# Performance work log

Hardware: AMD Instinct MI355X
Metric: run time of the kernel (lower is better)

## Reference

```python
import jax, jax.numpy as jnp
import numpy as np

N = 32768      # nodes
E = 262144     # edges
G = 256        # graphs
D_IN, D_H, D_OUT = 256, 512, 512
STEPS = 3      # set2set processing steps


def setup_inputs() -> dict:
    key = jax.random.key(0)
    ks = jax.random.split(key, 10)
    x = jax.random.normal(ks[0], (N, D_IN), jnp.float32)
    edge_index = jax.random.randint(ks[1], (2, E), 0, N, dtype=jnp.int64)
    batch = jnp.sort(jax.random.randint(ks[2], (N,), 0, G, dtype=jnp.int64))
    W1 = jax.random.normal(ks[3], (D_IN, D_H), jnp.float32) * (1.0 / np.sqrt(D_IN))
    b1 = jnp.zeros((D_H,), jnp.float32)
    W2 = jax.random.normal(ks[4], (D_H, D_OUT), jnp.float32) * (1.0 / np.sqrt(D_H))
    b2 = jnp.zeros((D_OUT,), jnp.float32)
    # LSTM(input=2*D_OUT, hidden=D_OUT); gate order i,f,g,o (PyTorch)
    s = 1.0 / np.sqrt(D_OUT)
    W_ih = jax.random.uniform(ks[5], (4 * D_OUT, 2 * D_OUT), jnp.float32, -s, s)
    W_hh = jax.random.uniform(ks[6], (4 * D_OUT, D_OUT), jnp.float32, -s, s)
    b_ih = jax.random.uniform(ks[7], (4 * D_OUT,), jnp.float32, -s, s)
    b_hh = jax.random.uniform(ks[8], (4 * D_OUT,), jnp.float32, -s, s)
    return {"x": x, "edge_index": edge_index, "batch": batch,
            "W1": W1, "b1": b1, "W2": W2, "b2": b2,
            "W_ih": W_ih, "W_hh": W_hh, "b_ih": b_ih, "b_hh": b_hh}


def _gcn_conv(x, src, dst, norm, W, b):
    # GCNConv: symmetric-normalized aggregation of linearly transformed features
    h = x @ W                              # [N, d_out]
    msg = h[src] * norm[:, None]           # gather + scale  [E+N, d_out]
    agg = jax.ops.segment_sum(msg, dst, num_segments=N)
    return agg + b


def reference(x, edge_index, batch, W1, b1, W2, b2, W_ih, W_hh, b_ih, b_hh):
    # --- GCN normalization with self-loops: D^-1/2 (A+I) D^-1/2 ---
    loop = jnp.arange(N, dtype=edge_index.dtype)
    src = jnp.concatenate([edge_index[0], loop])
    dst = jnp.concatenate([edge_index[1], loop])
    deg = jax.ops.segment_sum(jnp.ones_like(src, x.dtype), dst, num_segments=N)
    dinv = jax.lax.rsqrt(deg)              # deg >= 1 thanks to self-loops
    norm = dinv[src] * dinv[dst]

    h = jax.nn.relu(_gcn_conv(x, src, dst, norm, W1, b1))
    h = _gcn_conv(h, src, dst, norm, W2, b2)   # [N, D_OUT]

    # --- Set2Set pooling (3 processing steps) ---
    d = D_OUT
    q_star = jnp.zeros((G, 2 * d), h.dtype)
    hs = jnp.zeros((G, d), h.dtype)
    cs = jnp.zeros((G, d), h.dtype)
    for _ in range(STEPS):
        gates = q_star @ W_ih.T + b_ih + hs @ W_hh.T + b_hh
        i, f, g, o = jnp.split(gates, 4, axis=-1)
        cs = jax.nn.sigmoid(f) * cs + jax.nn.sigmoid(i) * jnp.tanh(g)
        hs = jax.nn.sigmoid(o) * jnp.tanh(cs)      # query q  [G, d]
        e = jnp.sum(h * hs[batch], axis=-1)        # [N]
        emax = jax.ops.segment_max(e, batch, num_segments=G)
        emax = jnp.where(jnp.isfinite(emax), emax, 0.0)
        ex = jnp.exp(e - emax[batch])
        denom = jax.ops.segment_sum(ex, batch, num_segments=G)
        a = ex / jnp.maximum(denom, 1e-12)[batch]  # per-graph softmax
        r = jax.ops.segment_sum(a[:, None] * h, batch, num_segments=G)
        q_star = jnp.concatenate([hs, r], axis=-1)  # [G, 2d]
    return q_star
```

## Files before the change

### kernel.cpp

```cpp
#include <hip/hip_runtime.h>
#include <math.h>

#define NN 32768
#define NE 262144
#define NG 256
#define DIN 256
#define DH 512
#define DOUT 512

typedef unsigned short u16;
typedef _Float16 f16;
typedef __attribute__((ext_vector_type(4))) _Float16 f16x4;
typedef __attribute__((ext_vector_type(8))) _Float16 f16x8;
typedef __attribute__((ext_vector_type(4))) float f32x4;

__device__ inline void split2h(float f, f16& h, f16& l) {
  h = (f16)f;
  l = (f16)(f - (float)h);
}

__device__ inline void gload16(const void* g, void* l) {
  __builtin_amdgcn_global_load_lds((const __attribute__((address_space(1))) unsigned int*)g,
                                   (__attribute__((address_space(3))) unsigned int*)l,
                                   16, 0, 0);
}


__global__ __launch_bounds__(128) void k_scanA(const int* __restrict__ counts,
                                               int* __restrict__ bsum) {
  int b = blockIdx.x, t = threadIdx.x;
  int v = counts[b * 128 + t];
  __shared__ int red[128];
  red[t] = v;
  __syncthreads();
#pragma unroll
  for (int o = 64; o > 0; o >>= 1) {
    if (t < o) red[t] += red[t + o];
    __syncthreads();
  }
  if (t == 0) bsum[b] = red[0];
}

__global__ __launch_bounds__(256) void k_scanB(const int* __restrict__ bsum,
                                               int* __restrict__ boff,
                                               int* __restrict__ offs) {
  __shared__ int s[256];
  int t = threadIdx.x;
  int v = bsum[t];
  s[t] = v;
  __syncthreads();
  for (int o = 1; o < 256; o <<= 1) {
    int add = (t >= o) ? s[t - o] : 0;
    __syncthreads();
    s[t] += add;
    __syncthreads();
  }
  boff[t] = s[t] - v;
  if (t == 255) offs[NN] = s[255];
}

__global__ __launch_bounds__(128) void k_scanC(const int* __restrict__ counts,
                                               const int* __restrict__ boff,
                                               int* __restrict__ offs,
                                               float* __restrict__ dinv) {
  int b = blockIdx.x, t = threadIdx.x;
  int v = counts[b * 128 + t];
  __shared__ int s[128];
  s[t] = v;
  __syncthreads();
  for (int o = 1; o < 128; o <<= 1) {
    int add = (t >= o) ? s[t - o] : 0;
    __syncthreads();
    s[t] += add;
    __syncthreads();
  }
  offs[b * 128 + t] = boff[b] + s[t] - v;
  dinv[b * 128 + t] = rsqrtf((float)(v + 1));
}

__global__ void k_fill(const int* __restrict__ ei, const int* __restrict__ offs,
                       int* __restrict__ cursor, int* __restrict__ csr) {
  int e = blockIdx.x * 256 + threadIdx.x;
  if (e < NE) {
    int d = ei[NE + e];
    int pos = offs[d] + atomicAdd(&cursor[d], 1);
    csr[pos] = ei[e];
  }
}

__global__ void k_prep(const float* __restrict__ x, f16* __restrict__ xh,
                       const float* __restrict__ W1, f16* __restrict__ w1th,
                       const float* __restrict__ W2, f16* __restrict__ w2th,
                       const float* __restrict__ W_ih, const float* __restrict__ W_hh,
                       f16* __restrict__ wgh,
                       const int* __restrict__ batch, int* __restrict__ starts,
                       const int* __restrict__ ei, int* __restrict__ counts) {
  int b = blockIdx.x;
  if (b < 8192) {
    int i = (b * 256 + threadIdx.x) << 2;
    float4 v = *(const float4*)(x + i);
    f16x4 h = {(f16)v.x, (f16)v.y, (f16)v.z, (f16)v.w};
    *(f16x4*)(xh + i) = h;
  } else if (b < 8704) {
    int idx = (b - 8192) * 256 + threadIdx.x;
    int k = idx >> 9, n = idx & 511;
    w1th[(size_t)n * DIN + k] = (f16)W1[idx];
  } else if (b < 9728) {
    int idx = (b - 8704) * 256 + threadIdx.x;
    int k = idx >> 9, n = idx & 511;
    w2th[(size_t)n * DH + k] = (f16)W2[idx];
  } else if (b < 17920) {
    int idx = (b - 9728) * 256 + threadIdx.x;
    int n = idx >> 10, c = idx & 1023;
    float v = W_ih[(size_t)n * 1024 + c];
    if (c < 512) v += W_hh[(size_t)n * 512 + c];
    wgh[idx] = (f16)v;
  } else if (b == 17920) {
    int g = threadIdx.x;
    int lo = 0, hi = NN;
    while (lo < hi) {
      int mid = (lo + hi) >> 1;
      if (batch[mid] < g) lo = mid + 1; else hi = mid;
    }
    starts[g] = lo;
    if (g == 0) starts[NG] = NN;
  } else {
    int e = (b - 17921) * 256 + threadIdx.x;
    if (e < NE) atomicAdd(&counts[ei[NE + e]], 1);
  }
}

template <int MODE, int TERMS>
__global__ __launch_bounds__(256) void k_mfma_gemm(
    const f16* __restrict__ Ahi, const f16* __restrict__ Alo,
    const f16* __restrict__ Bhi,
    float* __restrict__ C, f16* __restrict__ Cf16, const float* __restrict__ bias,
    int M, int N, int K, int lda, int ldb) {
  constexpr int BOFF = (TERMS == 2) ? 32768 : 16384;
  __shared__ char lds[(TERMS == 2) ? 49152 : 32768];

  int nbn = N >> 7;
  int nwg = (M >> 7) * nbn;
  int b = blockIdx.x;
  int slice = b / nwg;
  b -= slice * nwg;
  int koff = slice * K;
  int swz = (b & 7) * (nwg >> 3) + (b >> 3);
  int bn = (swz % nbn) << 7;
  int bm = (swz / nbn) << 7;

  int tid = threadIdx.x;
  int w = tid >> 6, lane = tid & 63;
  int wm = (w >> 1) << 6, wn = (w & 1) << 6;
  int fr = lane & 15;
  int fq = lane >> 4;

  f32x4 acc[4][4];
#pragma unroll
  for (int i = 0; i < 4; ++i)
#pragma unroll
    for (int j = 0; j < 4; ++j) acc[i][j] = (f32x4){0.f, 0.f, 0.f, 0.f};

  for (int ks = 0; ks < K; ks += 64) {
#pragma unroll
    for (int i = 0; i < 4; ++i) {
      int L = i * 256 + tid;
      int row = L >> 3;
      int ke = ((L & 7) ^ (row & 7)) << 3;
      int ldsoff = i * 4096 + w * 1024;
      gload16(Ahi + (size_t)(bm + row) * lda + koff + ks + ke, lds + ldsoff);
      if (TERMS == 2)
        gload16(Alo + (size_t)(bm + row) * lda + koff + ks + ke, lds + 16384 + ldsoff);
      gload16(Bhi + (size_t)(bn + row) * ldb + koff + ks + ke, lds + BOFF + ldsoff);
    }
    __syncthreads();
#pragma unroll
    for (int kk = 0; kk < 2; ++kk) {
      f16x8 ah[4], al[4], bh[4];
#pragma unroll
      for (int m = 0; m < 4; ++m) {
        int row = wm + m * 16 + fr;
        int boff = row * 128 + (((kk << 6) + (fq << 4)) ^ ((row & 7) << 4));
        ah[m] = *(const f16x8*)(lds + boff);
        if (TERMS == 2) al[m] = *(const f16x8*)(lds + 16384 + boff);
      }
#pragma unroll
      for (int n = 0; n < 4; ++n) {
        int row = wn + n * 16 + fr;
        int boff = row * 128 + (((kk << 6) + (fq << 4)) ^ ((row & 7) << 4));
        bh[n] = *(const f16x8*)(lds + BOFF + boff);
      }
#pragma unroll
      for (int m = 0; m < 4; ++m)
#pragma unroll
        for (int n = 0; n < 4; ++n) {
          acc[m][n] = __builtin_amdgcn_mfma_f32_16x16x32_f16(ah[m], bh[n], acc[m][n], 0, 0, 0);
          if (TERMS == 2)
            acc[m][n] = __builtin_amdgcn_mfma_f32_16x16x32_f16(al[m], bh[n], acc[m][n], 0, 0, 0);
        }
    }
    __syncthreads();
  }
#pragma unroll
  for (int m = 0; m < 4; ++m)
#pragma unroll
    for (int n = 0; n < 4; ++n)
#pragma unroll
      for (int i = 0; i < 4; ++i) {
        int r = bm + wm + m * 16 + fq * 4 + i;
        int c = bn + wn + n * 16 + fr;
        float val = acc[m][n][i];
        if (MODE == 1) {
          val += bias[c];
          val = fmaxf(val, 0.f);
          Cf16[(size_t)r * N + c] = (f16)val;
        } else if (MODE == 2) {
          Cf16[(size_t)r * N + c] = (f16)val;
        } else {
          C[(size_t)slice * M * N + (size_t)r * N + c] = val;
        }
      }
}

__global__ __launch_bounds__(256) void k_agg256(const f16* __restrict__ xh,
                                                const int* __restrict__ offs,
                                                const int* __restrict__ csr,
                                                const float* __restrict__ dinv,
                                                f16* __restrict__ oh) {
  int wv = threadIdx.x >> 6, lane = threadIdx.x & 63;
  int v = blockIdx.x * 4 + wv;
  int f = lane << 2;
  int s = offs[v], t = offs[v + 1];
  float dv = dinv[v];
  f16x4 rs = *(const f16x4*)(xh + (size_t)v * DIN + f);
  float a0[4] = {}, a1[4] = {}, a2[4] = {}, a3[4] = {};
  for (int base = s; base < t; base += 64) {
    int rem = min(64, t - base);
    int idx = (lane < rem) ? csr[base + lane] : 0;
    float wl = (lane < rem) ? dinv[idx] : 0.f;
    int i = 0;
    for (; i + 7 < rem; i += 8) {
      int u[8]; float ww[8]; f16x4 r[8];
#pragma unroll
      for (int q = 0; q < 8; ++q) { u[q] = __shfl(idx, i + q); ww[q] = __shfl(wl, i + q); }
#pragma unroll
      for (int q = 0; q < 8; ++q) r[q] = *(const f16x4*)(xh + (size_t)u[q] * DIN + f);
#pragma unroll
      for (int k = 0; k < 4; ++k) {
        a0[k] += ww[0] * (float)r[0][k]; a1[k] += ww[1] * (float)r[1][k];
        a2[k] += ww[2] * (float)r[2][k]; a3[k] += ww[3] * (float)r[3][k];
        a0[k] += ww[4] * (float)r[4][k]; a1[k] += ww[5] * (float)r[5][k];
        a2[k] += ww[6] * (float)r[6][k]; a3[k] += ww[7] * (float)r[7][k];
      }
    }
    for (; i + 1 < rem; i += 2) {
      int u0 = __shfl(idx, i), u1 = __shfl(idx, i + 1);
      float w0 = __shfl(wl, i), w1 = __shfl(wl, i + 1);
      f16x4 r0 = *(const f16x4*)(xh + (size_t)u0 * DIN + f);
      f16x4 r1 = *(const f16x4*)(xh + (size_t)u1 * DIN + f);
#pragma unroll
      for (int k = 0; k < 4; ++k) { a0[k] += w0 * (float)r0[k]; a1[k] += w1 * (float)r1[k]; }
    }
    if (i < rem) {
      int u0 = __shfl(idx, i);
      float w0 = __shfl(wl, i);
      f16x4 r0 = *(const f16x4*)(xh + (size_t)u0 * DIN + f);
#pragma unroll
      for (int k = 0; k < 4; ++k) a0[k] += w0 * (float)r0[k];
    }
  }
  f16x4 vh;
#pragma unroll
  for (int k = 0; k < 4; ++k)
    vh[k] = (f16)((a0[k] + a1[k] + a2[k] + a3[k] + dv * (float)rs[k]) * dv);
  *(f16x4*)(oh + (size_t)v * DIN + f) = vh;
}

__global__ __launch_bounds__(256) void k_agg512(const f16* __restrict__ T2,
                                                const int* __restrict__ offs,
                                                const int* __restrict__ csr,
                                                const float* __restrict__ dinv,
                                                const float* __restrict__ bias,
                                                f16* __restrict__ H2) {
  int half = blockIdx.x / (NN / 4);
  int blk = blockIdx.x - half * (NN / 4);
  int wv = threadIdx.x >> 6, lane = threadIdx.x & 63;
  int v = blk * 4 + wv;
  int f = half * 256 + (lane << 2);
  int s = offs[v], t = offs[v + 1];
  float dv = dinv[v];
  f16x4 rs = *(const f16x4*)(T2 + (size_t)v * DH + f);
  float a0[4] = {}, a1[4] = {}, a2[4] = {}, a3[4] = {};
  for (int base = s; base < t; base += 64) {
    int rem = min(64, t - base);
    int idx = (lane < rem) ? csr[base + lane] : 0;
    float wl = (lane < rem) ? dinv[idx] : 0.f;
    int i = 0;
    for (; i + 7 < rem; i += 8) {
      int u[8]; float ww[8]; f16x4 r[8];
#pragma unroll
      for (int q = 0; q < 8; ++q) { u[q] = __shfl(idx, i + q); ww[q] = __shfl(wl, i + q); }
#pragma unroll
      for (int q = 0; q < 8; ++q) r[q] = *(const f16x4*)(T2 + (size_t)u[q] * DH + f);
#pragma unroll
      for (int k = 0; k < 4; ++k) {
        a0[k] += ww[0] * (float)r[0][k]; a1[k] += ww[1] * (float)r[1][k];
        a2[k] += ww[2] * (float)r[2][k]; a3[k] += ww[3] * (float)r[3][k];
        a0[k] += ww[4] * (float)r[4][k]; a1[k] += ww[5] * (float)r[5][k];
        a2[k] += ww[6] * (float)r[6][k]; a3[k] += ww[7] * (float)r[7][k];
      }
    }
    for (; i + 1 < rem; i += 2) {
      int u0 = __shfl(idx, i), u1 = __shfl(idx, i + 1);
      float w0 = __shfl(wl, i), w1 = __shfl(wl, i + 1);
      f16x4 r0 = *(const f16x4*)(T2 + (size_t)u0 * DH + f);
      f16x4 r1 = *(const f16x4*)(T2 + (size_t)u1 * DH + f);
#pragma unroll
      for (int k = 0; k < 4; ++k) { a0[k] += w0 * (float)r0[k]; a1[k] += w1 * (float)r1[k]; }
    }
    if (i < rem) {
      int u0 = __shfl(idx, i);
      float w0 = __shfl(wl, i);
      f16x4 r0 = *(const f16x4*)(T2 + (size_t)u0 * DH + f);
#pragma unroll
      for (int k = 0; k < 4; ++k) a0[k] += w0 * (float)r0[k];
    }
  }
  float4 bb = *(const float4*)(bias + f);
  float bbv[4] = {bb.x, bb.y, bb.z, bb.w};
  f16x4 out;
#pragma unroll
  for (int k = 0; k < 4; ++k)
    out[k] = (f16)((a0[k] + a1[k] + a2[k] + a3[k] + dv * (float)rs[k]) * dv + bbv[k]);
  *(f16x4*)(H2 + (size_t)v * DH + f) = out;
}

template <int STEP0>
__global__ __launch_bounds__(512) void k_step(const float* __restrict__ gp,
                                              const float* __restrict__ b_ih,
                                              const float* __restrict__ b_hh,
                                              float* __restrict__ cs,
                                              const f16* __restrict__ H2,
                                              const int* __restrict__ starts,
                                              float* __restrict__ qstar,
                                              f16* __restrict__ qhhi, f16* __restrict__ qhlo) {
  int g = blockIdx.x;
  int tid = threadIdx.x, wv = tid >> 6, lane = tid & 63;
  __shared__ float shs[512];
  __shared__ float lm[8], lsum[8];
  __shared__ float lr[8][512];

  {
    int j = tid;
    float iv = b_ih[j]        + b_hh[j];
    float fv = b_ih[512 + j]  + b_hh[512 + j];
    float gv = b_ih[1024 + j] + b_hh[1024 + j];
    float ov = b_ih[1536 + j] + b_hh[1536 + j];
    if (!STEP0) {
      const float* g0 = gp + (size_t)g * 2048;
#pragma unroll
      for (int sl = 0; sl < 8; ++sl) {
        const float* gs = g0 + (size_t)sl * 524288;
        iv += gs[j]; fv += gs[512 + j]; gv += gs[1024 + j]; ov += gs[1536 + j];
      }
    }
    float si = 1.f / (1.f + expf(-iv));
    float sf = 1.f / (1.f + expf(-fv));
    float so = 1.f / (1.f + expf(-ov));
    float cprev = STEP0 ? 0.f : cs[(size_t)g * 512 + j];
    float c = sf * cprev + si * tanhf(gv);
    float h = so * tanhf(c);
    cs[(size_t)g * 512 + j] = c;
    shs[j] = h;
    qstar[(size_t)g * 1024 + j] = h;
    f16 hh, hl;
    split2h(h, hh, hl);
    qhhi[(size_t)g * 1024 + j] = hh;
    qhlo[(size_t)g * 1024 + j] = hl;
  }
  __syncthreads();

  int s = starts[g], t = starts[g + 1];
  int cnt = t - s;
  float hsr[8];
#pragma unroll
  for (int k = 0; k < 8; ++k) hsr[k] = shs[lane * 8 + k];

  float m = -INFINITY, ssum = 0.f;
  float racc[8] = {};
  f16x8 rv = {};
  if (wv < cnt) rv = *(const f16x8*)(H2 + (size_t)(s + wv) * DH + lane * 8);
  for (int i = wv; i < cnt; i += 8) {
    f16x8 cur = rv;
    if (i + 8 < cnt) rv = *(const f16x8*)(H2 + (size_t)(s + i + 8) * DH + lane * 8);
    float e = 0.f;
#pragma unroll
    for (int k = 0; k < 8; ++k) e += (float)cur[k] * hsr[k];
#pragma unroll
    for (int o = 1; o < 64; o <<= 1) e += __shfl_xor(e, o);
    float mn = fmaxf(m, e);
    float scale = expf(m - mn);
    float p = expf(e - mn);
    ssum = ssum * scale + p;
#pragma unroll
    for (int k = 0; k < 8; ++k) racc[k] = racc[k] * scale + p * (float)cur[k];
    m = mn;
  }
  if (lane == 0) { lm[wv] = m; lsum[wv] = ssum; }
#pragma unroll
  for (int k = 0; k < 8; ++k) lr[wv][lane * 8 + k] = racc[k];
  __syncthreads();
  float M = -INFINITY;
#pragma unroll
  for (int w2 = 0; w2 < 8; ++w2) M = fmaxf(M, lm[w2]);
  if (!(M > -3.0e38f)) M = 0.f;
  float denom = 0.f;
  float sc[8];
#pragma unroll
  for (int w2 = 0; w2 < 8; ++w2) { sc[w2] = expf(lm[w2] - M); denom += lsum[w2] * sc[w2]; }
  float inv = 1.f / fmaxf(denom, 1e-12f);
  int f = tid;
  float r = 0.f;
#pragma unroll
  for (int w2 = 0; w2 < 8; ++w2) r += lr[w2][f] * sc[w2];
  r *= inv;
  qstar[(size_t)g * 1024 + 512 + f] = r;
  f16 h0, l0;
  split2h(r, h0, l0);
  qhhi[(size_t)g * 1024 + 512 + f] = h0;
  qhlo[(size_t)g * 1024 + 512 + f] = l0;
}

extern "C" void kernel_launch(void* const* d_in, const int* in_sizes, int n_in,
                              void* d_out, int out_size, void* d_ws, size_t ws_size,
                              hipStream_t stream) {
  const float* x     = (const float*)d_in[0];
  const int*   ei    = (const int*)d_in[1];
  const int*   batch = (const int*)d_in[2];
  const float* W1    = (const float*)d_in[3];
  const float* b1    = (const float*)d_in[4];
  const float* W2    = (const float*)d_in[5];
  const float* b2    = (const float*)d_in[6];
  const float* W_ih  = (const float*)d_in[7];
  const float* W_hh  = (const float*)d_in[8];
  const float* b_ih  = (const float*)d_in[9];
  const float* b_hh  = (const float*)d_in[10];
  float* qstar = (float*)d_out;

  char* w = (char*)d_ws;
  size_t off = 0;
  auto carve = [&](size_t bytes) -> void* {
    void* p = w + off;
    off += (bytes + 255) & ~(size_t)255;
    return p;
  };
  f16* xh      = (f16*)carve((size_t)NN * DIN * 2);
  f16* axh     = (f16*)carve((size_t)NN * DIN * 2);
  f16* h1h     = (f16*)carve((size_t)NN * DH * 2);
  f16* t2h     = (f16*)carve((size_t)NN * DH * 2);
  f16* H2h     = (f16*)carve((size_t)NN * DH * 2);
  f16* w1th    = (f16*)carve((size_t)DH * DIN * 2);
  f16* w2th    = (f16*)carve((size_t)DH * DH * 2);
  f16* wgh     = (f16*)carve((size_t)2048 * 1024 * 2);
  float* gp    = (float*)carve((size_t)8 * NG * 2048 * 4);
  int* counts  = (int*)carve((size_t)NN * 4);
  int* cursor  = (int*)carve((size_t)NN * 4);
  float* cs    = (float*)carve((size_t)NG * DOUT * 4);
  f16* qhhi    = (f16*)carve((size_t)NG * 1024 * 2);
  f16* qhlo    = (f16*)carve((size_t)NG * 1024 * 2);
  int* offs    = (int*)carve((size_t)(NN + 1) * 4);
  int* csr     = (int*)carve((size_t)NE * 4);
  float* dinv  = (float*)carve((size_t)NN * 4);
  int* starts  = (int*)carve((size_t)(NG + 1) * 4);
  int* bsum    = (int*)carve((size_t)256 * 4);
  int* boff    = (int*)carve((size_t)256 * 4);

  hipMemsetAsync(counts, 0, (size_t)2 * NN * 4, stream);

  k_prep<<<18945, 256, 0, stream>>>(x, xh, W1, w1th, W2, w2th, W_ih, W_hh, wgh,
                                    batch, starts, ei, counts);
  k_scanA<<<NN / 128, 128, 0, stream>>>(counts, bsum);
  k_scanB<<<1, 256, 0, stream>>>(bsum, boff, offs);
  k_scanC<<<NN / 128, 128, 0, stream>>>(counts, boff, offs, dinv);
  k_fill<<<NE / 256, 256, 0, stream>>>(ei, offs, cursor, csr);

  k_agg256<<<NN / 4, 256, 0, stream>>>(xh, offs, csr, dinv, axh);
  k_mfma_gemm<1, 1><<<(NN / 128) * (DH / 128), 256, 0, stream>>>(
      axh, nullptr, w1th, nullptr, h1h, b1, NN, DH, DIN, DIN, DIN);
  k_mfma_gemm<2, 1><<<(NN / 128) * (DH / 128), 256, 0, stream>>>(
      h1h, nullptr, w2th, nullptr, t2h, nullptr, NN, DH, DH, DH, DH);
  k_agg512<<<NN / 2, 256, 0, stream>>>(t2h, offs, csr, dinv, b2, H2h);

  k_step<1><<<NG, 512, 0, stream>>>(nullptr, b_ih, b_hh, cs, H2h, starts, qstar, qhhi, qhlo);
  for (int step = 1; step < 3; ++step) {
    k_mfma_gemm<0, 2><<<8 * (NG / 128) * (2048 / 128), 256, 0, stream>>>(
        qhhi, qhlo, wgh, gp, nullptr, nullptr, NG, 2048, 128, 1024, 1024);
    k_step<0><<<NG, 512, 0, stream>>>(gp, b_ih, b_hh, cs, H2h, starts, qstar, qhhi, qhlo);
  }
}
```

Baseline: 223.9 us.

## Fuse Set2Set steps into one cooperative kernel and merge scan kernels

Replaces the five Set2Set launches (step kernels plus split-K gate GEMMs) with one cooperative kernel that uses grid-wide syncs, with all 256 blocks doing both the gate GEMM slice and the attention step. It also merges the three-kernel prefix scan into one kernel that recomputes each block's prefix by summing all earlier counts, and deepens the H2 prefetch to two rows. The aim is to cut launch overhead and small-kernel tails. In exchange it adds grid.sync cost, leaves half the threads idle in the GEMM phase, and makes the scan do redundant quadratic reads.

```diff
diff --git a/kernel.cpp b/kernel.cpp
--- a/kernel.cpp
+++ b/kernel.cpp
@@ -1,5 +1,8 @@
 #include <hip/hip_runtime.h>
+#include <hip/hip_cooperative_groups.h>
 #include <math.h>
+
+namespace cg = cooperative_groups;
 
 #define NN 32768
 #define NE 262144
@@ -23,69 +26,6 @@
   __builtin_amdgcn_global_load_lds((const __attribute__((address_space(1))) unsigned int*)g,
                                    (__attribute__((address_space(3))) unsigned int*)l,
                                    16, 0, 0);
-}
-
-
-__global__ __launch_bounds__(128) void k_scanA(const int* __restrict__ counts,
-                                               int* __restrict__ bsum) {
-  int b = blockIdx.x, t = threadIdx.x;
-  int v = counts[b * 128 + t];
-  __shared__ int red[128];
-  red[t] = v;
-  __syncthreads();
-#pragma unroll
-  for (int o = 64; o > 0; o >>= 1) {
-    if (t < o) red[t] += red[t + o];
-    __syncthreads();
-  }
-  if (t == 0) bsum[b] = red[0];
-}
-
-__global__ __launch_bounds__(256) void k_scanB(const int* __restrict__ bsum,
-                                               int* __restrict__ boff,
-                                               int* __restrict__ offs) {
-  __shared__ int s[256];
-  int t = threadIdx.x;
-  int v = bsum[t];
-  s[t] = v;
-  __syncthreads();
-  for (int o = 1; o < 256; o <<= 1) {
-    int add = (t >= o) ? s[t - o] : 0;
-    __syncthreads();
-    s[t] += add;
-    __syncthreads();
-  }
-  boff[t] = s[t] - v;
-  if (t == 255) offs[NN] = s[255];
-}
-
-__global__ __launch_bounds__(128) void k_scanC(const int* __restrict__ counts,
-                                               const int* __restrict__ boff,
-                                               int* __restrict__ offs,
-                                               float* __restrict__ dinv) {
-  int b = blockIdx.x, t = threadIdx.x;
-  int v = counts[b * 128 + t];
-  __shared__ int s[128];
-  s[t] = v;
-  __syncthreads();
-  for (int o = 1; o < 128; o <<= 1) {
-    int add = (t >= o) ? s[t - o] : 0;
-    __syncthreads();
-    s[t] += add;
-    __syncthreads();
-  }
-  offs[b * 128 + t] = boff[b] + s[t] - v;
-  dinv[b * 128 + t] = rsqrtf((float)(v + 1));
-}
-
-__global__ void k_fill(const int* __restrict__ ei, const int* __restrict__ offs,
-                       int* __restrict__ cursor, int* __restrict__ csr) {
-  int e = blockIdx.x * 256 + threadIdx.x;
-  if (e < NE) {
-    int d = ei[NE + e];
-    int pos = offs[d] + atomicAdd(&cursor[d], 1);
-    csr[pos] = ei[e];
-  }
 }
 
 __global__ void k_prep(const float* __restrict__ x, f16* __restrict__ xh,
@@ -130,21 +70,60 @@
   }
 }
 
-template <int MODE, int TERMS>
+__global__ __launch_bounds__(256) void k_scan_all(const int* __restrict__ counts,
+                                                  int* __restrict__ offs,
+                                                  float* __restrict__ dinv) {
+  int b = blockIdx.x, tid = threadIdx.x;
+  int limit = b * 128;
+  __shared__ int red[256];
+  int ssum = 0;
+  for (int i = tid; i < limit; i += 256) ssum += counts[i];
+  red[tid] = ssum;
+  __syncthreads();
+#pragma unroll
+  for (int o = 128; o > 0; o >>= 1) {
+    if (tid < o) red[tid] += red[tid + o];
+    __syncthreads();
+  }
+  int prefix = red[0];
+  __syncthreads();
+  __shared__ int s[128];
+  int v = 0;
+  if (tid < 128) { v = counts[limit + tid]; s[tid] = v; }
+  __syncthreads();
+  for (int o = 1; o < 128; o <<= 1) {
+    int add = (tid >= o && tid < 128) ? s[tid - o] : 0;
+    __syncthreads();
+    if (tid < 128) s[tid] += add;
+    __syncthreads();
+  }
+  if (tid < 128) {
+    offs[limit + tid] = prefix + s[tid] - v;
+    dinv[limit + tid] = rsqrtf((float)(v + 1));
+  }
+  if (b == 255 && tid == 127) offs[NN] = prefix + s[127];
+}
+
+__global__ void k_fill(const int* __restrict__ ei, const int* __restrict__ offs,
+                       int* __restrict__ cursor, int* __restrict__ csr) {
+  int e = blockIdx.x * 256 + threadIdx.x;
+  if (e < NE) {
+    int d = ei[NE + e];
+    int pos = offs[d] + atomicAdd(&cursor[d], 1);
+    csr[pos] = ei[e];
+  }
+}
+
+template <int MODE>
 __global__ __launch_bounds__(256) void k_mfma_gemm(
-    const f16* __restrict__ Ahi, const f16* __restrict__ Alo,
-    const f16* __restrict__ Bhi,
-    float* __restrict__ C, f16* __restrict__ Cf16, const float* __restrict__ bias,
+    const f16* __restrict__ A, const f16* __restrict__ B,
+    f16* __restrict__ Cf16, const float* __restrict__ bias,
     int M, int N, int K, int lda, int ldb) {
-  constexpr int BOFF = (TERMS == 2) ? 32768 : 16384;
-  __shared__ char lds[(TERMS == 2) ? 49152 : 32768];
+  __shared__ char lds[32768];
 
   int nbn = N >> 7;
   int nwg = (M >> 7) * nbn;
   int b = blockIdx.x;
-  int slice = b / nwg;
-  b -= slice * nwg;
-  int koff = slice * K;
   int swz = (b & 7) * (nwg >> 3) + (b >> 3);
   int bn = (swz % nbn) << 7;
   int bm = (swz / nbn) << 7;
@@ -168,36 +147,30 @@
       int row = L >> 3;
       int ke = ((L & 7) ^ (row & 7)) << 3;
       int ldsoff = i * 4096 + w * 1024;
-      gload16(Ahi + (size_t)(bm + row) * lda + koff + ks + ke, lds + ldsoff);
-      if (TERMS == 2)
-        gload16(Alo + (size_t)(bm + row) * lda + koff + ks + ke, lds + 16384 + ldsoff);
-      gload16(Bhi + (size_t)(bn + row) * ldb + koff + ks + ke, lds + BOFF + ldsoff);
+      gload16(A + (size_t)(bm + row) * lda + ks + ke, lds + ldsoff);
+      gload16(B + (size_t)(bn + row) * ldb + ks + ke, lds + 16384 + ldsoff);
     }
     __syncthreads();
 #pragma unroll
     for (int kk = 0; kk < 2; ++kk) {
-      f16x8 ah[4], al[4], bh[4];
+      f16x8 ah[4], bh[4];
 #pragma unroll
       for (int m = 0; m < 4; ++m) {
         int row = wm + m * 16 + fr;
         int boff = row * 128 + (((kk << 6) + (fq << 4)) ^ ((row & 7) << 4));
         ah[m] = *(const f16x8*)(lds + boff);
-        if (TERMS == 2) al[m] = *(const f16x8*)(lds + 16384 + boff);
       }
 #pragma unroll
       for (int n = 0; n < 4; ++n) {
         int row = wn + n * 16 + fr;
         int boff = row * 128 + (((kk << 6) + (fq << 4)) ^ ((row & 7) << 4));
-        bh[n] = *(const f16x8*)(lds + BOFF + boff);
+        bh[n] = *(const f16x8*)(lds + 16384 + boff);
       }
 #pragma unroll
       for (int m = 0; m < 4; ++m)
 #pragma unroll
-        for (int n = 0; n < 4; ++n) {
+        for (int n = 0; n < 4; ++n)
           acc[m][n] = __builtin_amdgcn_mfma_f32_16x16x32_f16(ah[m], bh[n], acc[m][n], 0, 0, 0);
-          if (TERMS == 2)
-            acc[m][n] = __builtin_amdgcn_mfma_f32_16x16x32_f16(al[m], bh[n], acc[m][n], 0, 0, 0);
-        }
     }
     __syncthreads();
   }
@@ -213,12 +186,8 @@
         if (MODE == 1) {
           val += bias[c];
           val = fmaxf(val, 0.f);
-          Cf16[(size_t)r * N + c] = (f16)val;
-        } else if (MODE == 2) {
-          Cf16[(size_t)r * N + c] = (f16)val;
-        } else {
-          C[(size_t)slice * M * N + (size_t)r * N + c] = val;
         }
+        Cf16[(size_t)r * N + c] = (f16)val;
       }
 }
 
@@ -335,100 +304,186 @@
   *(f16x4*)(H2 + (size_t)v * DH + f) = out;
 }
 
-template <int STEP0>
-__global__ __launch_bounds__(512) void k_step(const float* __restrict__ gp,
-                                              const float* __restrict__ b_ih,
-                                              const float* __restrict__ b_hh,
-                                              float* __restrict__ cs,
-                                              const f16* __restrict__ H2,
-                                              const int* __restrict__ starts,
-                                              float* __restrict__ qstar,
-                                              f16* __restrict__ qhhi, f16* __restrict__ qhlo) {
+__global__ __launch_bounds__(512) void k_set2set(
+    const float* __restrict__ b_ih, const float* __restrict__ b_hh,
+    float* __restrict__ cs, const f16* __restrict__ H2,
+    const int* __restrict__ starts, float* __restrict__ qstar,
+    f16* __restrict__ qhhi, f16* __restrict__ qhlo,
+    const f16* __restrict__ wgh, float* __restrict__ gp) {
+  cg::grid_group grid = cg::this_grid();
   int g = blockIdx.x;
   int tid = threadIdx.x, wv = tid >> 6, lane = tid & 63;
-  __shared__ float shs[512];
-  __shared__ float lm[8], lsum[8];
-  __shared__ float lr[8][512];
-
-  {
-    int j = tid;
-    float iv = b_ih[j]        + b_hh[j];
-    float fv = b_ih[512 + j]  + b_hh[512 + j];
-    float gv = b_ih[1024 + j] + b_hh[1024 + j];
-    float ov = b_ih[1536 + j] + b_hh[1536 + j];
-    if (!STEP0) {
-      const float* g0 = gp + (size_t)g * 2048;
-#pragma unroll
-      for (int sl = 0; sl < 8; ++sl) {
-        const float* gs = g0 + (size_t)sl * 524288;
-        iv += gs[j]; fv += gs[512 + j]; gv += gs[1024 + j]; ov += gs[1536 + j];
-      }
-    }
-    float si = 1.f / (1.f + expf(-iv));
-    float sf = 1.f / (1.f + expf(-fv));
-    float so = 1.f / (1.f + expf(-ov));
-    float cprev = STEP0 ? 0.f : cs[(size_t)g * 512 + j];
-    float c = sf * cprev + si * tanhf(gv);
-    float h = so * tanhf(c);
-    cs[(size_t)g * 512 + j] = c;
-    shs[j] = h;
-    qstar[(size_t)g * 1024 + j] = h;
-    f16 hh, hl;
-    split2h(h, hh, hl);
-    qhhi[(size_t)g * 1024 + j] = hh;
-    qhlo[(size_t)g * 1024 + j] = hl;
-  }
-  __syncthreads();
-
-  int s = starts[g], t = starts[g + 1];
-  int cnt = t - s;
-  float hsr[8];
-#pragma unroll
-  for (int k = 0; k < 8; ++k) hsr[k] = shs[lane * 8 + k];
-
-  float m = -INFINITY, ssum = 0.f;
-  float racc[8] = {};
-  f16x8 rv = {};
-  if (wv < cnt) rv = *(const f16x8*)(H2 + (size_t)(s + wv) * DH + lane * 8);
-  for (int i = wv; i < cnt; i += 8) {
-    f16x8 cur = rv;
-    if (i + 8 < cnt) rv = *(const f16x8*)(H2 + (size_t)(s + i + 8) * DH + lane * 8);
-    float e = 0.f;
-#pragma unroll
-    for (int k = 0; k < 8; ++k) e += (float)cur[k] * hsr[k];
-#pragma unroll
-    for (int o = 1; o < 64; o <<= 1) e += __shfl_xor(e, o);
-    float mn = fmaxf(m, e);
-    float scale = expf(m - mn);
-    float p = expf(e - mn);
-    ssum = ssum * scale + p;
-#pragma unroll
-    for (int k = 0; k < 8; ++k) racc[k] = racc[k] * scale + p * (float)cur[k];
-    m = mn;
-  }
-  if (lane == 0) { lm[wv] = m; lsum[wv] = ssum; }
-#pragma unroll
-  for (int k = 0; k < 8; ++k) lr[wv][lane * 8 + k] = racc[k];
-  __syncthreads();
-  float M = -INFINITY;
-#pragma unroll
-  for (int w2 = 0; w2 < 8; ++w2) M = fmaxf(M, lm[w2]);
-  if (!(M > -3.0e38f)) M = 0.f;
-  float denom = 0.f;
-  float sc[8];
-#pragma unroll
-  for (int w2 = 0; w2 < 8; ++w2) { sc[w2] = expf(lm[w2] - M); denom += lsum[w2] * sc[w2]; }
-  float inv = 1.f / fmaxf(denom, 1e-12f);
-  int f = tid;
-  float r = 0.f;
-#pragma unroll
-  for (int w2 = 0; w2 < 8; ++w2) r += lr[w2][f] * sc[w2];
-  r *= inv;
-  qstar[(size_t)g * 1024 + 512 + f] = r;
-  f16 h0, l0;
-  split2h(r, h0, l0);
-  qhhi[(size_t)g * 1024 + 512 + f] = h0;
-  qhlo[(size_t)g * 1024 + 512 + f] = l0;
+  __shared__ __align__(16) char smem[49152];
+  float* shs = (float*)smem;
+  float* lr = (float*)(smem + 2048);
+  float* lm = (float*)(smem + 2048 + 16384);
+  float* lsum = lm + 8;
+
+  for (int it = 0; it < 3; ++it) {
+    if (it > 0) {
+      __threadfence();
+      grid.sync();
+      {
+        const int nbn = 16, nwg = 32;
+        int b = blockIdx.x;
+        int slice = b / nwg;
+        int bb = b - slice * nwg;
+        int koff = slice * 128;
+        int swz = (bb & 7) * (nwg >> 3) + (bb >> 3);
+        int bn = (swz % nbn) << 7;
+        int bm = (swz / nbn) << 7;
+        int w = tid >> 6;
+        int wm = (w >> 1) << 6, wn = (w & 1) << 6;
+        int fr = lane & 15, fq = lane >> 4;
+        f32x4 acc[4][4];
+#pragma unroll
+        for (int i = 0; i < 4; ++i)
+#pragma unroll
+          for (int j = 0; j < 4; ++j) acc[i][j] = (f32x4){0.f, 0.f, 0.f, 0.f};
+        for (int ks = 0; ks < 128; ks += 64) {
+          if (tid < 256) {
+#pragma unroll
+            for (int i = 0; i < 4; ++i) {
+              int L = i * 256 + tid;
+              int row = L >> 3;
+              int ke = ((L & 7) ^ (row & 7)) << 3;
+              int ldsoff = i * 4096 + w * 1024;
+              gload16(qhhi + (size_t)(bm + row) * 1024 + koff + ks + ke, smem + ldsoff);
+              gload16(qhlo + (size_t)(bm + row) * 1024 + koff + ks + ke, smem + 16384 + ldsoff);
+              gload16(wgh + (size_t)(bn + row) * 1024 + koff + ks + ke, smem + 32768 + ldsoff);
+            }
+          }
+          __syncthreads();
+          if (tid < 256) {
+#pragma unroll
+            for (int kk = 0; kk < 2; ++kk) {
+              f16x8 ah[4], al[4], bh[4];
+#pragma unroll
+              for (int m = 0; m < 4; ++m) {
+                int row = wm + m * 16 + fr;
+                int boff = row * 128 + (((kk << 6) + (fq << 4)) ^ ((row & 7) << 4));
+                ah[m] = *(const f16x8*)(smem + boff);
+                al[m] = *(const f16x8*)(smem + 16384 + boff);
+              }
+#pragma unroll
+              for (int n = 0; n < 4; ++n) {
+                int row = wn + n * 16 + fr;
+                int boff = row * 128 + (((kk << 6) + (fq << 4)) ^ ((row & 7) << 4));
+                bh[n] = *(const f16x8*)(smem + 32768 + boff);
+              }
+#pragma unroll
+              for (int m = 0; m < 4; ++m)
+#pragma unroll
+                for (int n = 0; n < 4; ++n) {
+                  acc[m][n] = __builtin_amdgcn_mfma_f32_16x16x32_f16(ah[m], bh[n], acc[m][n], 0, 0, 0);
+                  acc[m][n] = __builtin_amdgcn_mfma_f32_16x16x32_f16(al[m], bh[n], acc[m][n], 0, 0, 0);
+                }
+            }
+          }
+          __syncthreads();
+        }
+        if (tid < 256) {
+#pragma unroll
+          for (int m = 0; m < 4; ++m)
+#pragma unroll
+            for (int n = 0; n < 4; ++n)
+#pragma unroll
+              for (int i = 0; i < 4; ++i) {
+                int r = bm + wm + m * 16 + fq * 4 + i;
+                int c = bn + wn + n * 16 + fr;
+                gp[(size_t)slice * 524288 + (size_t)r * 2048 + c] = acc[m][n][i];
+              }
+        }
+      }
+      __threadfence();
+      grid.sync();
+    }
+
+    {
+      int j = tid;
+      float iv = b_ih[j]        + b_hh[j];
+      float fv = b_ih[512 + j]  + b_hh[512 + j];
+      float gv = b_ih[1024 + j] + b_hh[1024 + j];
+      float ov = b_ih[1536 + j] + b_hh[1536 + j];
+      if (it > 0) {
+        const float* g0 = gp + (size_t)g * 2048;
+#pragma unroll
+        for (int sl = 0; sl < 8; ++sl) {
+          const float* gs = g0 + (size_t)sl * 524288;
+          iv += gs[j]; fv += gs[512 + j]; gv += gs[1024 + j]; ov += gs[1536 + j];
+        }
+      }
+      float si = 1.f / (1.f + expf(-iv));
+      float sf = 1.f / (1.f + expf(-fv));
+      float so = 1.f / (1.f + expf(-ov));
+      float cprev = (it == 0) ? 0.f : cs[(size_t)g * 512 + j];
+      float c = sf * cprev + si * tanhf(gv);
+      float h = so * tanhf(c);
+      cs[(size_t)g * 512 + j] = c;
+      shs[j] = h;
+      qstar[(size_t)g * 1024 + j] = h;
+      f16 hh, hl;
+      split2h(h, hh, hl);
+      qhhi[(size_t)g * 1024 + j] = hh;
+      qhlo[(size_t)g * 1024 + j] = hl;
+    }
+    __syncthreads();
+
+    {
+      int s = starts[g], t = starts[g + 1];
+      int cnt = t - s;
+      float hsr[8];
+#pragma unroll
+      for (int k = 0; k < 8; ++k) hsr[k] = shs[lane * 8 + k];
+
+      float m = -INFINITY, ssum = 0.f;
+      float racc[8] = {};
+      f16x8 rv0 = {}, rv1 = {};
+      if (wv < cnt) rv0 = *(const f16x8*)(H2 + (size_t)(s + wv) * DH + lane * 8);
+      if (wv + 8 < cnt) rv1 = *(const f16x8*)(H2 + (size_t)(s + wv + 8) * DH + lane * 8);
+      for (int i = wv; i < cnt; i += 8) {
+        f16x8 cur = rv0;
+        rv0 = rv1;
+        if (i + 16 < cnt) rv1 = *(const f16x8*)(H2 + (size_t)(s + i + 16) * DH + lane * 8);
+        float e = 0.f;
+#pragma unroll
+        for (int k = 0; k < 8; ++k) e += (float)cur[k] * hsr[k];
+#pragma unroll
+        for (int o = 1; o < 64; o <<= 1) e += __shfl_xor(e, o);
+        float mn = fmaxf(m, e);
+        float scale = expf(m - mn);
+        float p = expf(e - mn);
+        ssum = ssum * scale + p;
+#pragma unroll
+        for (int k = 0; k < 8; ++k) racc[k] = racc[k] * scale + p * (float)cur[k];
+        m = mn;
+      }
+      if (lane == 0) { lm[wv] = m; lsum[wv] = ssum; }
+#pragma unroll
+      for (int k = 0; k < 8; ++k) lr[wv * 512 + lane * 8 + k] = racc[k];
+      __syncthreads();
+      float M = -INFINITY;
+#pragma unroll
+      for (int w2 = 0; w2 < 8; ++w2) M = fmaxf(M, lm[w2]);
+      if (!(M > -3.0e38f)) M = 0.f;
+      float denom = 0.f;
+      float sc[8];
+#pragma unroll
+      for (int w2 = 0; w2 < 8; ++w2) { sc[w2] = expf(lm[w2] - M); denom += lsum[w2] * sc[w2]; }
+      float inv = 1.f / fmaxf(denom, 1e-12f);
+      int f = tid;
+      float r = 0.f;
+#pragma unroll
+      for (int w2 = 0; w2 < 8; ++w2) r += lr[w2 * 512 + f] * sc[w2];
+      r *= inv;
+      qstar[(size_t)g * 1024 + 512 + f] = r;
+      f16 h0, l0;
+      split2h(r, h0, l0);
+      qhhi[(size_t)g * 1024 + 512 + f] = h0;
+      qhlo[(size_t)g * 1024 + 512 + f] = l0;
+    }
+    __syncthreads();
+  }
 }
 
 extern "C" void kernel_launch(void* const* d_in, const int* in_sizes, int n_in,
@@ -472,29 +527,22 @@
   int* csr     = (int*)carve((size_t)NE * 4);
   float* dinv  = (float*)carve((size_t)NN * 4);
   int* starts  = (int*)carve((size_t)(NG + 1) * 4);
-  int* bsum    = (int*)carve((size_t)256 * 4);
-  int* boff    = (int*)carve((size_t)256 * 4);
 
   hipMemsetAsync(counts, 0, (size_t)2 * NN * 4, stream);
 
   k_prep<<<18945, 256, 0, stream>>>(x, xh, W1, w1th, W2, w2th, W_ih, W_hh, wgh,
                                     batch, starts, ei, counts);
-  k_scanA<<<NN / 128, 128, 0, stream>>>(counts, bsum);
-  k_scanB<<<1, 256, 0, stream>>>(bsum, boff, offs);
-  k_scanC<<<NN / 128, 128, 0, stream>>>(counts, boff, offs, dinv);
+  k_scan_all<<<256, 256, 0, stream>>>(counts, offs, dinv);
   k_fill<<<NE / 256, 256, 0, stream>>>(ei, offs, cursor, csr);
 
   k_agg256<<<NN / 4, 256, 0, stream>>>(xh, offs, csr, dinv, axh);
-  k_mfma_gemm<1, 1><<<(NN / 128) * (DH / 128), 256, 0, stream>>>(
-      axh, nullptr, w1th, nullptr, h1h, b1, NN, DH, DIN, DIN, DIN);
-  k_mfma_gemm<2, 1><<<(NN / 128) * (DH / 128), 256, 0, stream>>>(
-      h1h, nullptr, w2th, nullptr, t2h, nullptr, NN, DH, DH, DH, DH);
+  k_mfma_gemm<1><<<(NN / 128) * (DH / 128), 256, 0, stream>>>(
+      axh, w1th, h1h, b1, NN, DH, DIN, DIN, DIN);
+  k_mfma_gemm<2><<<(NN / 128) * (DH / 128), 256, 0, stream>>>(
+      h1h, w2th, t2h, nullptr, NN, DH, DH, DH, DH);
   k_agg512<<<NN / 2, 256, 0, stream>>>(t2h, offs, csr, dinv, b2, H2h);
 
-  k_step<1><<<NG, 512, 0, stream>>>(nullptr, b_ih, b_hh, cs, H2h, starts, qstar, qhhi, qhlo);
-  for (int step = 1; step < 3; ++step) {
-    k_mfma_gemm<0, 2><<<8 * (NG / 128) * (2048 / 128), 256, 0, stream>>>(
-        qhhi, qhlo, wgh, gp, nullptr, nullptr, NG, 2048, 128, 1024, 1024);
-    k_step<0><<<NG, 512, 0, stream>>>(gp, b_ih, b_hh, cs, H2h, starts, qstar, qhhi, qhlo);
-  }
-}
+  void* args[] = {(void*)&b_ih, (void*)&b_hh, (void*)&cs, (void*)&H2h, (void*)&starts,
+                  (void*)&qstar, (void*)&qhhi, (void*)&qhlo, (void*)&wgh, (void*)&gp};
+  hipLaunchCooperativeKernel((void*)k_set2set, dim3(NG), dim3(512), args, 0, stream);
+}
```

Result: slower. 520.6 us (+132.5%).
